# Kernel optimization log

Hardware: AMD Instinct MI355X
Metric: run time of the kernel (lower is better)

Reference implementation:

```python
import jax, jax.numpy as jnp
import numpy as np

SOBEL_X = jnp.array([[1., 0., -1.], [2., 0., -2.], [1., 0., -1.]], dtype=jnp.float32).reshape(1, 1, 3, 3)
SOBEL_Y = jnp.array([[1., 2., 1.], [0., 0., 0.], [-1., -2., -1.]], dtype=jnp.float32).reshape(1, 1, 3, 3)
EPS = 1e-3


def _sobel(img, kern):
    # img: [N, 1, H, W]; 3x3 conv, zero padding 1 (torch Conv2d padding=1)
    return jax.lax.conv_general_dilated(
        img, kern, window_strides=(1, 1), padding='SAME',
        dimension_numbers=('NCHW', 'OIHW', 'NCHW'))


def _compute_flow(frames):
    # frames: [B, T, 3, H, W] -> flow: [B, T-1, 2, H, W]
    B, T, C, H, W = frames.shape
    gray = (0.2989 * frames[:, :, 0] + 0.587 * frames[:, :, 1]
            + 0.114 * frames[:, :, 2])  # [B, T, H, W]
    I1 = gray[:, :-1].reshape(B * (T - 1), 1, H, W)
    I2 = gray[:, 1:].reshape(B * (T - 1), 1, H, W)
    Ix = _sobel(I1, SOBEL_X)
    Iy = _sobel(I1, SOBEL_Y)
    It = I2 - I1
    denom = Ix * Ix + Iy * Iy + EPS
    u = -Ix * It / denom
    v = -Iy * It / denom
    return jnp.concatenate([u, v], axis=1).reshape(B, T - 1, 2, H, W)


def setup_inputs() -> dict:
    key = jax.random.key(0)
    k1, k2 = jax.random.split(key)
    shape = (8, 8, 3, 256, 256)  # [B, T, C, H, W]
    pred = jax.random.uniform(k1, shape, dtype=jnp.float32)
    gt = jax.random.uniform(k2, shape, dtype=jnp.float32)
    return {"pred": pred, "gt": gt}


def reference(pred, gt):
    pred_flow = _compute_flow(pred)  # [B, T-1, 2, H, W]
    gt_flow = _compute_flow(gt)
    # motion magnitude: mean abs frame diff over channels, broadcast over 2 flow channels
    motion_mag = jnp.abs(gt[:, 1:] - gt[:, :-1]).mean(axis=2, keepdims=True)  # [B, T-1, 1, H, W]
    flow_loss = (jnp.abs(pred_flow - gt_flow) * motion_mag).mean()
    return flow_loss
```

## Files before the change

kernel.cpp:

```cpp
#include <hip/hip_runtime.h>

#define BB 8
#define TT 8
#define CC 3
#define HH 256
#define WW 256
#define PAIRS (BB * (TT - 1))
#define TX 32
#define TY 8
#define TILES_X (WW / TX)
#define TILES_Y (HH / TY)
#define NBLOCKS (PAIRS * TILES_X * TILES_Y)
#define FRAME_PIX (HH * WW)
#define EPS 1e-3f

#define INV_N (1.0f / (float)((size_t)PAIRS * 2 * HH * WW))

__global__ __launch_bounds__(TX * TY) void flow_loss_kernel(
    const float* __restrict__ pred, const float* __restrict__ gt,
    float* __restrict__ partial)
{
    __shared__ float sp[TY + 2][TX + 2];
    __shared__ float sg[TY + 2][TX + 2];

    const int pair = blockIdx.z;
    const int b = pair / (TT - 1);
    const int t = pair % (TT - 1);

    const size_t frame_stride = (size_t)CC * FRAME_PIX;
    const float* p1 = pred + ((size_t)b * TT + t) * frame_stride;
    const float* p2 = p1 + frame_stride;
    const float* g1 = gt + ((size_t)b * TT + t) * frame_stride;
    const float* g2 = g1 + frame_stride;

    const int x0 = blockIdx.x * TX - 1;
    const int y0 = blockIdx.y * TY - 1;
    const int tid = threadIdx.y * TX + threadIdx.x;

    for (int i = tid; i < (TX + 2) * (TY + 2); i += TX * TY) {
        const int lx = i % (TX + 2);
        const int ly = i / (TX + 2);
        const int gx = x0 + lx;
        const int gy = y0 + ly;
        float vp = 0.0f, vg = 0.0f;
        if ((unsigned)gx < WW && (unsigned)gy < HH) {
            const int idx = gy * WW + gx;
            vp = 0.2989f * p1[idx] + 0.587f * p1[idx + FRAME_PIX]
               + 0.114f * p1[idx + 2 * FRAME_PIX];
            vg = 0.2989f * g1[idx] + 0.587f * g1[idx + FRAME_PIX]
               + 0.114f * g1[idx + 2 * FRAME_PIX];
        }
        sp[ly][lx] = vp;
        sg[ly][lx] = vg;
    }
    __syncthreads();

    const int gx = blockIdx.x * TX + threadIdx.x;
    const int gy = blockIdx.y * TY + threadIdx.y;
    const int idx = gy * WW + gx;

    const float p2r = p2[idx], p2g = p2[idx + FRAME_PIX], p2b = p2[idx + 2 * FRAME_PIX];
    const float g2r = g2[idx], g2g = g2[idx + FRAME_PIX], g2b = g2[idx + 2 * FRAME_PIX];
    const float g1r = g1[idx], g1g = g1[idx + FRAME_PIX], g1b = g1[idx + 2 * FRAME_PIX];

    const float gray_p2 = 0.2989f * p2r + 0.587f * p2g + 0.114f * p2b;
    const float gray_g2 = 0.2989f * g2r + 0.587f * g2g + 0.114f * g2b;
    const float mm = (fabsf(g2r - g1r) + fabsf(g2g - g1g) + fabsf(g2b - g1b)) * (1.0f / 3.0f);

    const int lx = threadIdx.x + 1;
    const int ly = threadIdx.y + 1;

    float a00 = sp[ly - 1][lx - 1], a01 = sp[ly - 1][lx], a02 = sp[ly - 1][lx + 1];
    float a10 = sp[ly    ][lx - 1], a11 = sp[ly    ][lx], a12 = sp[ly    ][lx + 1];
    float a20 = sp[ly + 1][lx - 1], a21 = sp[ly + 1][lx], a22 = sp[ly + 1][lx + 1];
    float Ix = (a00 - a02) + 2.0f * (a10 - a12) + (a20 - a22);
    float Iy = (a00 + 2.0f * a01 + a02) - (a20 + 2.0f * a21 + a22);
    float It = gray_p2 - a11;
    float d  = Ix * Ix + Iy * Iy + EPS;
    float up = -(Ix * It) / d;
    float vp = -(Iy * It) / d;

    a00 = sg[ly - 1][lx - 1]; a01 = sg[ly - 1][lx]; a02 = sg[ly - 1][lx + 1];
    a10 = sg[ly    ][lx - 1]; a11 = sg[ly    ][lx]; a12 = sg[ly    ][lx + 1];
    a20 = sg[ly + 1][lx - 1]; a21 = sg[ly + 1][lx]; a22 = sg[ly + 1][lx + 1];
    Ix = (a00 - a02) + 2.0f * (a10 - a12) + (a20 - a22);
    Iy = (a00 + 2.0f * a01 + a02) - (a20 + 2.0f * a21 + a22);
    It = gray_g2 - a11;
    d  = Ix * Ix + Iy * Iy + EPS;
    const float ug = -(Ix * It) / d;
    const float vg = -(Iy * It) / d;

    float s = (fabsf(up - ug) + fabsf(vp - vg)) * mm;

    #pragma unroll
    for (int off = 32; off > 0; off >>= 1) s += __shfl_down(s, off, 64);

    __shared__ float wsum[TX * TY / 64];
    if ((tid & 63) == 0) wsum[tid >> 6] = s;
    __syncthreads();
    if (tid == 0) {
        float bs = 0.0f;
        #pragma unroll
        for (int w = 0; w < TX * TY / 64; ++w) bs += wsum[w];
        partial[(blockIdx.z * TILES_Y + blockIdx.y) * TILES_X + blockIdx.x] = bs;
    }
}

__global__ __launch_bounds__(256) void reduce_kernel(
    const float* __restrict__ partial, float* __restrict__ out)
{
    float s = 0.0f;
    for (int i = threadIdx.x; i < NBLOCKS; i += 256) s += partial[i];
    #pragma unroll
    for (int off = 32; off > 0; off >>= 1) s += __shfl_down(s, off, 64);

    __shared__ float wsum[4];
    if ((threadIdx.x & 63) == 0) wsum[threadIdx.x >> 6] = s;
    __syncthreads();
    if (threadIdx.x == 0) {
        out[0] = (wsum[0] + wsum[1] + wsum[2] + wsum[3]) * INV_N;
    }
}

extern "C" void kernel_launch(void* const* d_in, const int* in_sizes, int n_in,
                              void* d_out, int out_size, void* d_ws, size_t ws_size,
                              hipStream_t stream) {
    const float* pred = (const float*)d_in[0];
    const float* gt   = (const float*)d_in[1];
    float* partial    = (float*)d_ws;
    float* out        = (float*)d_out;

    dim3 grid(TILES_X, TILES_Y, PAIRS);
    dim3 block(TX, TY);
    flow_loss_kernel<<<grid, block, 0, stream>>>(pred, gt, partial);
    reduce_kernel<<<1, 256, 0, stream>>>(partial, out);
}
```

Before: 144.9 us.

## Use full-width row tiles with float4 loads and four pixels per thread

```diff
diff --git a/kernel.cpp b/kernel.cpp
--- a/kernel.cpp
+++ b/kernel.cpp
@@ -2,107 +2,138 @@
 
 #define BB 8
 #define TT 8
-#define CC 3
 #define HH 256
 #define WW 256
 #define PAIRS (BB * (TT - 1))
-#define TX 32
-#define TY 8
-#define TILES_X (WW / TX)
-#define TILES_Y (HH / TY)
-#define NBLOCKS (PAIRS * TILES_X * TILES_Y)
 #define FRAME_PIX (HH * WW)
+#define RROWS 8
+#define HROWS (RROWS + 2)
+#define PADW 264
+#define NY (HH / RROWS)
+#define NBLK (PAIRS * NY)
 #define EPS 1e-3f
-
 #define INV_N (1.0f / (float)((size_t)PAIRS * 2 * HH * WW))
 
-__global__ __launch_bounds__(TX * TY) void flow_loss_kernel(
+__device__ __forceinline__ float4 ld4(const float* __restrict__ p) {
+    return *reinterpret_cast<const float4*>(p);
+}
+
+__global__ __launch_bounds__(256) void flow_loss_kernel(
     const float* __restrict__ pred, const float* __restrict__ gt,
     float* __restrict__ partial)
 {
-    __shared__ float sp[TY + 2][TX + 2];
-    __shared__ float sg[TY + 2][TX + 2];
+    __shared__ float sg[2][HROWS][PADW];
 
-    const int pair = blockIdx.z;
+    const int ytile = blockIdx.x;
+    const int pair  = blockIdx.y;
     const int b = pair / (TT - 1);
     const int t = pair % (TT - 1);
+    const size_t fs = (size_t)3 * FRAME_PIX;
+    const float* p1 = pred + ((size_t)b * TT + t) * fs;
+    const float* p2 = p1 + fs;
+    const float* g1 = gt + ((size_t)b * TT + t) * fs;
+    const float* g2 = g1 + fs;
 
-    const size_t frame_stride = (size_t)CC * FRAME_PIX;
-    const float* p1 = pred + ((size_t)b * TT + t) * frame_stride;
-    const float* p2 = p1 + frame_stride;
-    const float* g1 = gt + ((size_t)b * TT + t) * frame_stride;
-    const float* g2 = g1 + frame_stride;
+    const int y0 = ytile * RROWS;
+    const int tid = threadIdx.x;
 
-    const int x0 = blockIdx.x * TX - 1;
-    const int y0 = blockIdx.y * TY - 1;
-    const int tid = threadIdx.y * TX + threadIdx.x;
-
-    for (int i = tid; i < (TX + 2) * (TY + 2); i += TX * TY) {
-        const int lx = i % (TX + 2);
-        const int ly = i / (TX + 2);
-        const int gx = x0 + lx;
-        const int gy = y0 + ly;
-        float vp = 0.0f, vg = 0.0f;
-        if ((unsigned)gx < WW && (unsigned)gy < HH) {
-            const int idx = gy * WW + gx;
-            vp = 0.2989f * p1[idx] + 0.587f * p1[idx + FRAME_PIX]
-               + 0.114f * p1[idx + 2 * FRAME_PIX];
-            vg = 0.2989f * g1[idx] + 0.587f * g1[idx + FRAME_PIX]
-               + 0.114f * g1[idx + 2 * FRAME_PIX];
+    for (int i = tid; i < 2 * HROWS * 66; i += 256) {
+        const int img = i / (HROWS * 66);
+        const int rem = i - img * (HROWS * 66);
+        const int row = rem / 66;
+        const int p   = rem - row * 66;
+        const int yr  = y0 - 1 + row;
+        float vx = 0.f, vy = 0.f, vz = 0.f, vw = 0.f;
+        if (p >= 1 && p <= 64 && (unsigned)yr < HH) {
+            const float* base = img ? g1 : p1;
+            const int off = yr * WW + (p - 1) * 4;
+            const float4 r  = ld4(base + off);
+            const float4 g  = ld4(base + off + FRAME_PIX);
+            const float4 bl = ld4(base + off + 2 * FRAME_PIX);
+            vx = 0.2989f * r.x + 0.587f * g.x + 0.114f * bl.x;
+            vy = 0.2989f * r.y + 0.587f * g.y + 0.114f * bl.y;
+            vz = 0.2989f * r.z + 0.587f * g.z + 0.114f * bl.z;
+            vw = 0.2989f * r.w + 0.587f * g.w + 0.114f * bl.w;
         }
-        sp[ly][lx] = vp;
-        sg[ly][lx] = vg;
+        float4 v; v.x = vx; v.y = vy; v.z = vz; v.w = vw;
+        *reinterpret_cast<float4*>(&sg[img][row][p * 4]) = v;
     }
     __syncthreads();
 
-    const int gx = blockIdx.x * TX + threadIdx.x;
-    const int gy = blockIdx.y * TY + threadIdx.y;
-    const int idx = gy * WW + gx;
+    const int c4 = tid & 63;
+    const int rb = tid >> 6;
+    const int x  = c4 * 4;
+    float s = 0.f;
 
-    const float p2r = p2[idx], p2g = p2[idx + FRAME_PIX], p2b = p2[idx + 2 * FRAME_PIX];
-    const float g2r = g2[idx], g2g = g2[idx + FRAME_PIX], g2b = g2[idx + 2 * FRAME_PIX];
-    const float g1r = g1[idx], g1g = g1[idx + FRAME_PIX], g1b = g1[idx + 2 * FRAME_PIX];
+    #pragma unroll
+    for (int pass = 0; pass < 2; ++pass) {
+        const int r   = pass * 4 + rb;
+        const int y   = y0 + r;
+        const int idx = y * WW + x;
 
-    const float gray_p2 = 0.2989f * p2r + 0.587f * p2g + 0.114f * p2b;
-    const float gray_g2 = 0.2989f * g2r + 0.587f * g2g + 0.114f * g2b;
-    const float mm = (fabsf(g2r - g1r) + fabsf(g2g - g1g) + fabsf(g2b - g1b)) * (1.0f / 3.0f);
+        const float4 ar = ld4(g1 + idx), ag = ld4(g1 + idx + FRAME_PIX), ab = ld4(g1 + idx + 2 * FRAME_PIX);
+        const float4 br = ld4(g2 + idx), bg = ld4(g2 + idx + FRAME_PIX), bb = ld4(g2 + idx + 2 * FRAME_PIX);
+        const float4 cr = ld4(p2 + idx), cg = ld4(p2 + idx + FRAME_PIX), cb = ld4(p2 + idx + 2 * FRAME_PIX);
 
-    const int lx = threadIdx.x + 1;
-    const int ly = threadIdx.y + 1;
+        float gp2[4], gg2[4], mm[4];
+        gp2[0] = 0.2989f * cr.x + 0.587f * cg.x + 0.114f * cb.x;
+        gp2[1] = 0.2989f * cr.y + 0.587f * cg.y + 0.114f * cb.y;
+        gp2[2] = 0.2989f * cr.z + 0.587f * cg.z + 0.114f * cb.z;
+        gp2[3] = 0.2989f * cr.w + 0.587f * cg.w + 0.114f * cb.w;
+        gg2[0] = 0.2989f * br.x + 0.587f * bg.x + 0.114f * bb.x;
+        gg2[1] = 0.2989f * br.y + 0.587f * bg.y + 0.114f * bb.y;
+        gg2[2] = 0.2989f * br.z + 0.587f * bg.z + 0.114f * bb.z;
+        gg2[3] = 0.2989f * br.w + 0.587f * bg.w + 0.114f * bb.w;
+        mm[0] = (fabsf(br.x - ar.x) + fabsf(bg.x - ag.x) + fabsf(bb.x - ab.x)) * (1.0f / 3.0f);
+        mm[1] = (fabsf(br.y - ar.y) + fabsf(bg.y - ag.y) + fabsf(bb.y - ab.y)) * (1.0f / 3.0f);
+        mm[2] = (fabsf(br.z - ar.z) + fabsf(bg.z - ag.z) + fabsf(bb.z - ab.z)) * (1.0f / 3.0f);
+        mm[3] = (fabsf(br.w - ar.w) + fabsf(bg.w - ag.w) + fabsf(bb.w - ab.w)) * (1.0f / 3.0f);
 
-    float a00 = sp[ly - 1][lx - 1], a01 = sp[ly - 1][lx], a02 = sp[ly - 1][lx + 1];
-    float a10 = sp[ly    ][lx - 1], a11 = sp[ly    ][lx], a12 = sp[ly    ][lx + 1];
-    float a20 = sp[ly + 1][lx - 1], a21 = sp[ly + 1][lx], a22 = sp[ly + 1][lx + 1];
-    float Ix = (a00 - a02) + 2.0f * (a10 - a12) + (a20 - a22);
-    float Iy = (a00 + 2.0f * a01 + a02) - (a20 + 2.0f * a21 + a22);
-    float It = gray_p2 - a11;
-    float d  = Ix * Ix + Iy * Iy + EPS;
-    float up = -(Ix * It) / d;
-    float vp = -(Iy * It) / d;
-
-    a00 = sg[ly - 1][lx - 1]; a01 = sg[ly - 1][lx]; a02 = sg[ly - 1][lx + 1];
-    a10 = sg[ly    ][lx - 1]; a11 = sg[ly    ][lx]; a12 = sg[ly    ][lx + 1];
-    a20 = sg[ly + 1][lx - 1]; a21 = sg[ly + 1][lx]; a22 = sg[ly + 1][lx + 1];
-    Ix = (a00 - a02) + 2.0f * (a10 - a12) + (a20 - a22);
-    Iy = (a00 + 2.0f * a01 + a02) - (a20 + 2.0f * a21 + a22);
-    It = gray_g2 - a11;
-    d  = Ix * Ix + Iy * Iy + EPS;
-    const float ug = -(Ix * It) / d;
-    const float vg = -(Iy * It) / d;
-
-    float s = (fabsf(up - ug) + fabsf(vp - vg)) * mm;
+        float up[4], vp[4];
+        #pragma unroll
+        for (int img = 0; img < 2; ++img) {
+            float w0[6], w1[6], w2[6];
+            {
+                const float* b0 = &sg[img][r][x];
+                const float4 A = ld4(b0), B = ld4(b0 + 4), C = ld4(b0 + 8);
+                w0[0] = A.w; w0[1] = B.x; w0[2] = B.y; w0[3] = B.z; w0[4] = B.w; w0[5] = C.x;
+            }
+            {
+                const float* b1 = &sg[img][r + 1][x];
+                const float4 A = ld4(b1), B = ld4(b1 + 4), C = ld4(b1 + 8);
+                w1[0] = A.w; w1[1] = B.x; w1[2] = B.y; w1[3] = B.z; w1[4] = B.w; w1[5] = C.x;
+            }
+            {
+                const float* b2 = &sg[img][r + 2][x];
+                const float4 A = ld4(b2), B = ld4(b2 + 4), C = ld4(b2 + 8);
+                w2[0] = A.w; w2[1] = B.x; w2[2] = B.y; w2[3] = B.z; w2[4] = B.w; w2[5] = C.x;
+            }
+            #pragma unroll
+            for (int j = 0; j < 4; ++j) {
+                const float Ix = (w0[j] - w0[j + 2]) + 2.0f * (w1[j] - w1[j + 2]) + (w2[j] - w2[j + 2]);
+                const float Iy = (w0[j] + 2.0f * w0[j + 1] + w0[j + 2])
+                               - (w2[j] + 2.0f * w2[j + 1] + w2[j + 2]);
+                const float It = (img ? gg2[j] : gp2[j]) - w1[j + 1];
+                const float d  = Ix * Ix + Iy * Iy + EPS;
+                const float inv = 1.0f / d;
+                if (img == 0) {
+                    up[j] = -(Ix * It) * inv;
+                    vp[j] = -(Iy * It) * inv;
+                } else {
+                    s += (fabsf(up[j] + (Ix * It) * inv) + fabsf(vp[j] + (Iy * It) * inv)) * mm[j];
+                }
+            }
+        }
+    }
 
     #pragma unroll
     for (int off = 32; off > 0; off >>= 1) s += __shfl_down(s, off, 64);
 
-    __shared__ float wsum[TX * TY / 64];
+    __shared__ float wsum[4];
     if ((tid & 63) == 0) wsum[tid >> 6] = s;
     __syncthreads();
     if (tid == 0) {
-        float bs = 0.0f;
-        #pragma unroll
-        for (int w = 0; w < TX * TY / 64; ++w) bs += wsum[w];
-        partial[(blockIdx.z * TILES_Y + blockIdx.y) * TILES_X + blockIdx.x] = bs;
+        partial[pair * NY + ytile] = wsum[0] + wsum[1] + wsum[2] + wsum[3];
     }
 }
 
@@ -110,7 +141,10 @@
     const float* __restrict__ partial, float* __restrict__ out)
 {
     float s = 0.0f;
-    for (int i = threadIdx.x; i < NBLOCKS; i += 256) s += partial[i];
+    for (int i = threadIdx.x; i < NBLK / 4; i += 256) {
+        const float4 v = ld4(partial + 4 * i);
+        s += (v.x + v.y) + (v.z + v.w);
+    }
     #pragma unroll
     for (int off = 32; off > 0; off >>= 1) s += __shfl_down(s, off, 64);
 
@@ -130,8 +164,8 @@
     float* partial    = (float*)d_ws;
     float* out        = (float*)d_out;
 
-    dim3 grid(TILES_X, TILES_Y, PAIRS);
-    dim3 block(TX, TY);
+    dim3 grid(NY, PAIRS);
+    dim3 block(256);
     flow_loss_kernel<<<grid, block, 0, stream>>>(pred, gt, partial);
     reduce_kernel<<<1, 256, 0, stream>>>(partial, out);
 }
```

After: 128.4 us. 1.13x faster.

## Replace shared-memory tiles with per-wave row bands using float4 loads and shuffles

Applied to the files above, without the earlier changes.

```diff
diff --git a/kernel.cpp b/kernel.cpp
--- a/kernel.cpp
+++ b/kernel.cpp
@@ -2,124 +2,168 @@
 
 #define BB 8
 #define TT 8
-#define CC 3
 #define HH 256
 #define WW 256
-#define PAIRS (BB * (TT - 1))
-#define TX 32
-#define TY 8
-#define TILES_X (WW / TX)
-#define TILES_Y (HH / TY)
-#define NBLOCKS (PAIRS * TILES_X * TILES_Y)
 #define FRAME_PIX (HH * WW)
+#define R_BAND 4
+#define NBANDS (HH / R_BAND)
+#define NPAIR (BB * (TT - 1))
+#define NITEM (NPAIR * NBANDS)
+#define NBLK (NITEM / 4)
 #define EPS 1e-3f
+#define INV_N (1.0f / (float)((size_t)NPAIR * 2 * HH * WW))
 
-#define INV_N (1.0f / (float)((size_t)PAIRS * 2 * HH * WW))
+__device__ __forceinline__ float4 ld4(const float* __restrict__ p) {
+    return *reinterpret_cast<const float4*>(p);
+}
+__device__ __forceinline__ float4 gray4(const float4 r, const float4 g, const float4 b) {
+    float4 o;
+    o.x = 0.2989f * r.x + 0.587f * g.x + 0.114f * b.x;
+    o.y = 0.2989f * r.y + 0.587f * g.y + 0.114f * b.y;
+    o.z = 0.2989f * r.z + 0.587f * g.z + 0.114f * b.z;
+    o.w = 0.2989f * r.w + 0.587f * g.w + 0.114f * b.w;
+    return o;
+}
 
-__global__ __launch_bounds__(TX * TY) void flow_loss_kernel(
+struct GrayRow { float4 g; float L, R; };
+
+__device__ __forceinline__ GrayRow make_row(const float4 r, const float4 g,
+                                            const float4 b, const int lane) {
+    GrayRow o;
+    o.g = gray4(r, g, b);
+    const float up = __shfl_up(o.g.w, 1, 64);
+    const float dn = __shfl_down(o.g.x, 1, 64);
+    o.L = (lane == 0)  ? 0.f : up;
+    o.R = (lane == 63) ? 0.f : dn;
+    return o;
+}
+
+__device__ __forceinline__ void sobel_uv(const GrayRow& wt, const GrayRow& wm,
+                                         const GrayRow& wb, const float4 g2v,
+                                         float* __restrict__ u, float* __restrict__ v) {
+    const float t_[6] = {wt.L, wt.g.x, wt.g.y, wt.g.z, wt.g.w, wt.R};
+    const float m_[6] = {wm.L, wm.g.x, wm.g.y, wm.g.z, wm.g.w, wm.R};
+    const float b_[6] = {wb.L, wb.g.x, wb.g.y, wb.g.z, wb.g.w, wb.R};
+    const float g2a[4] = {g2v.x, g2v.y, g2v.z, g2v.w};
+    #pragma unroll
+    for (int c = 0; c < 4; ++c) {
+        const float Ix = (t_[c] - t_[c + 2]) + 2.f * (m_[c] - m_[c + 2]) + (b_[c] - b_[c + 2]);
+        const float Iy = (t_[c] + 2.f * t_[c + 1] + t_[c + 2])
+                       - (b_[c] + 2.f * b_[c + 1] + b_[c + 2]);
+        const float It = g2a[c] - m_[c + 1];
+        const float inv = 1.f / (Ix * Ix + Iy * Iy + EPS);
+        u[c] = -(Ix * It) * inv;
+        v[c] = -(Iy * It) * inv;
+    }
+}
+
+__global__ __launch_bounds__(256, 3) void flow_loss_kernel(
     const float* __restrict__ pred, const float* __restrict__ gt,
     float* __restrict__ partial)
 {
-    __shared__ float sp[TY + 2][TX + 2];
-    __shared__ float sg[TY + 2][TX + 2];
+    const int tid   = threadIdx.x;
+    const int lane  = tid & 63;
+    const int witem = blockIdx.x * 4 + (tid >> 6);
+    const int pair  = witem >> 6;
+    const int band  = witem & (NBANDS - 1);
+    const int b     = pair / (TT - 1);
+    const int t     = pair % (TT - 1);
 
-    const int pair = blockIdx.z;
-    const int b = pair / (TT - 1);
-    const int t = pair % (TT - 1);
+    const size_t fs = (size_t)3 * FRAME_PIX;
+    const float* pt = pred + ((size_t)b * TT + t) * fs;
+    const float* p2 = pt + fs;
+    const float* g1 = gt + ((size_t)b * TT + t) * fs;
+    const float* g2 = g1 + fs;
 
-    const size_t frame_stride = (size_t)CC * FRAME_PIX;
-    const float* p1 = pred + ((size_t)b * TT + t) * frame_stride;
-    const float* p2 = p1 + frame_stride;
-    const float* g1 = gt + ((size_t)b * TT + t) * frame_stride;
-    const float* g2 = g1 + frame_stride;
+    const int y0 = band * R_BAND;
+    int off = (y0 - 1) * WW + lane * 4;
 
-    const int x0 = blockIdx.x * TX - 1;
-    const int y0 = blockIdx.y * TY - 1;
-    const int tid = threadIdx.y * TX + threadIdx.x;
+    GrayRow wp0, wp1, wp2, wg0, wg1, wg2;
+    float4 c1r, c1g, c1b;
 
-    for (int i = tid; i < (TX + 2) * (TY + 2); i += TX * TY) {
-        const int lx = i % (TX + 2);
-        const int ly = i / (TX + 2);
-        const int gx = x0 + lx;
-        const int gy = y0 + ly;
-        float vp = 0.0f, vg = 0.0f;
-        if ((unsigned)gx < WW && (unsigned)gy < HH) {
-            const int idx = gy * WW + gx;
-            vp = 0.2989f * p1[idx] + 0.587f * p1[idx + FRAME_PIX]
-               + 0.114f * p1[idx + 2 * FRAME_PIX];
-            vg = 0.2989f * g1[idx] + 0.587f * g1[idx + FRAME_PIX]
-               + 0.114f * g1[idx + 2 * FRAME_PIX];
+    {
+        float4 ar = {0,0,0,0}, ag = ar, ab_ = ar, br = ar, bg = ar, bb_ = ar;
+        if (y0 > 0) {
+            ar = ld4(pt + off); ag = ld4(pt + off + FRAME_PIX); ab_ = ld4(pt + off + 2 * FRAME_PIX);
+            br = ld4(g1 + off); bg = ld4(g1 + off + FRAME_PIX); bb_ = ld4(g1 + off + 2 * FRAME_PIX);
         }
-        sp[ly][lx] = vp;
-        sg[ly][lx] = vg;
+        wp0 = make_row(ar, ag, ab_, lane);
+        wg0 = make_row(br, bg, bb_, lane);
     }
-    __syncthreads();
+    off += WW;
+    {
+        const float4 ar = ld4(pt + off), ag = ld4(pt + off + FRAME_PIX),
+                     ab_ = ld4(pt + off + 2 * FRAME_PIX);
+        c1r = ld4(g1 + off); c1g = ld4(g1 + off + FRAME_PIX); c1b = ld4(g1 + off + 2 * FRAME_PIX);
+        wp1 = make_row(ar, ag, ab_, lane);
+        wg1 = make_row(c1r, c1g, c1b, lane);
+    }
+    off += WW;
 
-    const int gx = blockIdx.x * TX + threadIdx.x;
-    const int gy = blockIdx.y * TY + threadIdx.y;
-    const int idx = gy * WW + gx;
+    float s = 0.f;
+    #pragma unroll
+    for (int j = 0; j < R_BAND; ++j) {
+        const int y = y0 + j;
+        const bool vld = (y + 1) < HH;
 
-    const float p2r = p2[idx], p2g = p2[idx + FRAME_PIX], p2b = p2[idx + 2 * FRAME_PIX];
-    const float g2r = g2[idx], g2g = g2[idx + FRAME_PIX], g2b = g2[idx + 2 * FRAME_PIX];
-    const float g1r = g1[idx], g1g = g1[idx + FRAME_PIX], g1b = g1[idx + 2 * FRAME_PIX];
+        float4 ar = {0,0,0,0}, ag = ar, ab_ = ar, br = ar, bg = ar, bb_ = ar;
+        if (vld) {
+            ar = ld4(pt + off); ag = ld4(pt + off + FRAME_PIX); ab_ = ld4(pt + off + 2 * FRAME_PIX);
+            br = ld4(g1 + off); bg = ld4(g1 + off + FRAME_PIX); bb_ = ld4(g1 + off + 2 * FRAME_PIX);
+        }
+        const int off2 = off - WW;
+        const float4 pr2 = ld4(p2 + off2), pg2 = ld4(p2 + off2 + FRAME_PIX),
+                     pb2 = ld4(p2 + off2 + 2 * FRAME_PIX);
+        const float4 gr2 = ld4(g2 + off2), gg2c = ld4(g2 + off2 + FRAME_PIX),
+                     gb2 = ld4(g2 + off2 + 2 * FRAME_PIX);
 
-    const float gray_p2 = 0.2989f * p2r + 0.587f * p2g + 0.114f * p2b;
-    const float gray_g2 = 0.2989f * g2r + 0.587f * g2g + 0.114f * g2b;
-    const float mm = (fabsf(g2r - g1r) + fabsf(g2g - g1g) + fabsf(g2b - g1b)) * (1.0f / 3.0f);
+        wp2 = make_row(ar, ag, ab_, lane);
+        wg2 = make_row(br, bg, bb_, lane);
+        const float4 gp2v = gray4(pr2, pg2, pb2);
+        const float4 gg2v = gray4(gr2, gg2c, gb2);
 
-    const int lx = threadIdx.x + 1;
-    const int ly = threadIdx.y + 1;
+        float mm[4];
+        mm[0] = (fabsf(gr2.x - c1r.x) + fabsf(gg2c.x - c1g.x) + fabsf(gb2.x - c1b.x)) * (1.f / 3.f);
+        mm[1] = (fabsf(gr2.y - c1r.y) + fabsf(gg2c.y - c1g.y) + fabsf(gb2.y - c1b.y)) * (1.f / 3.f);
+        mm[2] = (fabsf(gr2.z - c1r.z) + fabsf(gg2c.z - c1g.z) + fabsf(gb2.z - c1b.z)) * (1.f / 3.f);
+        mm[3] = (fabsf(gr2.w - c1r.w) + fabsf(gg2c.w - c1g.w) + fabsf(gb2.w - c1b.w)) * (1.f / 3.f);
 
-    float a00 = sp[ly - 1][lx - 1], a01 = sp[ly - 1][lx], a02 = sp[ly - 1][lx + 1];
-    float a10 = sp[ly    ][lx - 1], a11 = sp[ly    ][lx], a12 = sp[ly    ][lx + 1];
-    float a20 = sp[ly + 1][lx - 1], a21 = sp[ly + 1][lx], a22 = sp[ly + 1][lx + 1];
-    float Ix = (a00 - a02) + 2.0f * (a10 - a12) + (a20 - a22);
-    float Iy = (a00 + 2.0f * a01 + a02) - (a20 + 2.0f * a21 + a22);
-    float It = gray_p2 - a11;
-    float d  = Ix * Ix + Iy * Iy + EPS;
-    float up = -(Ix * It) / d;
-    float vp = -(Iy * It) / d;
+        float up[4], vp[4], ug[4], vg[4];
+        sobel_uv(wp0, wp1, wp2, gp2v, up, vp);
+        sobel_uv(wg0, wg1, wg2, gg2v, ug, vg);
+        #pragma unroll
+        for (int c = 0; c < 4; ++c)
+            s += (fabsf(up[c] - ug[c]) + fabsf(vp[c] - vg[c])) * mm[c];
 
-    a00 = sg[ly - 1][lx - 1]; a01 = sg[ly - 1][lx]; a02 = sg[ly - 1][lx + 1];
-    a10 = sg[ly    ][lx - 1]; a11 = sg[ly    ][lx]; a12 = sg[ly    ][lx + 1];
-    a20 = sg[ly + 1][lx - 1]; a21 = sg[ly + 1][lx]; a22 = sg[ly + 1][lx + 1];
-    Ix = (a00 - a02) + 2.0f * (a10 - a12) + (a20 - a22);
-    Iy = (a00 + 2.0f * a01 + a02) - (a20 + 2.0f * a21 + a22);
-    It = gray_g2 - a11;
-    d  = Ix * Ix + Iy * Iy + EPS;
-    const float ug = -(Ix * It) / d;
-    const float vg = -(Iy * It) / d;
-
-    float s = (fabsf(up - ug) + fabsf(vp - vg)) * mm;
+        wp0 = wp1; wp1 = wp2; wg0 = wg1; wg1 = wg2;
+        c1r = br; c1g = bg; c1b = bb_;
+        off += WW;
+    }
 
     #pragma unroll
-    for (int off = 32; off > 0; off >>= 1) s += __shfl_down(s, off, 64);
+    for (int o = 32; o > 0; o >>= 1) s += __shfl_down(s, o, 64);
 
-    __shared__ float wsum[TX * TY / 64];
-    if ((tid & 63) == 0) wsum[tid >> 6] = s;
+    __shared__ float wsum[4];
+    if (lane == 0) wsum[tid >> 6] = s;
     __syncthreads();
-    if (tid == 0) {
-        float bs = 0.0f;
-        #pragma unroll
-        for (int w = 0; w < TX * TY / 64; ++w) bs += wsum[w];
-        partial[(blockIdx.z * TILES_Y + blockIdx.y) * TILES_X + blockIdx.x] = bs;
-    }
+    if (tid == 0)
+        partial[blockIdx.x] = (wsum[0] + wsum[1]) + (wsum[2] + wsum[3]);
 }
 
 __global__ __launch_bounds__(256) void reduce_kernel(
     const float* __restrict__ partial, float* __restrict__ out)
 {
-    float s = 0.0f;
-    for (int i = threadIdx.x; i < NBLOCKS; i += 256) s += partial[i];
+    const int i = threadIdx.x;
+    float s = partial[i] + partial[i + 256] + partial[i + 512];
+    if (i < NBLK - 768) s += partial[i + 768];
     #pragma unroll
-    for (int off = 32; off > 0; off >>= 1) s += __shfl_down(s, off, 64);
+    for (int o = 32; o > 0; o >>= 1) s += __shfl_down(s, o, 64);
 
     __shared__ float wsum[4];
-    if ((threadIdx.x & 63) == 0) wsum[threadIdx.x >> 6] = s;
+    if ((i & 63) == 0) wsum[i >> 6] = s;
     __syncthreads();
-    if (threadIdx.x == 0) {
-        out[0] = (wsum[0] + wsum[1] + wsum[2] + wsum[3]) * INV_N;
-    }
+    if (i == 0)
+        out[0] = ((wsum[0] + wsum[1]) + (wsum[2] + wsum[3])) * INV_N;
 }
 
 extern "C" void kernel_launch(void* const* d_in, const int* in_sizes, int n_in,
@@ -130,8 +174,6 @@
     float* partial    = (float*)d_ws;
     float* out        = (float*)d_out;
 
-    dim3 grid(TILES_X, TILES_Y, PAIRS);
-    dim3 block(TX, TY);
-    flow_loss_kernel<<<grid, block, 0, stream>>>(pred, gt, partial);
-    reduce_kernel<<<1, 256, 0, stream>>>(partial, out);
+    flow_loss_kernel<<<dim3(NBLK), dim3(256), 0, stream>>>(pred, gt, partial);
+    reduce_kernel<<<dim3(1), dim3(256), 0, stream>>>(partial, out);
 }
```

New measurement: 167.1 us. 15.3% more time.
